# Kernel optimization log

Measured on AMD Instinct MI355X. Metric: run time of the kernel, lower is better.

## Reference

```python
import jax, jax.numpy as jnp
import numpy as np
import math

B, N, D, H, E, EDGE_DIM, GEO_DIM = 32, 256, 512, 8, 1024, 256, 64
HD = D // H

def _lin(x, W, b):
    return x @ W.T + b

def _ln(x, g, b):
    m = x.mean(-1, keepdims=True)
    v = ((x - m) ** 2).mean(-1, keepdims=True)
    return (x - m) * jax.lax.rsqrt(v + 1e-5) * g + b

def setup_inputs() -> dict:
    key = jax.random.key(0)
    ks = jax.random.split(key, 20)
    p = lambda k, s: jax.random.normal(k, s, jnp.float32) * 0.02
    inp = {
        'x': jax.random.normal(ks[0], (B, N, D), jnp.float32),
        'node_masks': jnp.ones((B, N), jnp.float32),
        'relation_edges': jax.random.randint(ks[1], (B, E, 2), 0, N),
        'relation_masks': (jax.random.uniform(ks[2], (B, E)) > 0.2).astype(jnp.float32),
        'relation_embeddings': jax.random.normal(ks[3], (B, E, EDGE_DIM), jnp.float32),
        'relation_geo_features': jax.random.normal(ks[4], (B, E, GEO_DIM), jnp.float32),
        'Wq': p(ks[5], (D, D)), 'bq': jnp.zeros((D,), jnp.float32),
        'Wk': p(ks[6], (D, D)), 'bk': jnp.zeros((D,), jnp.float32),
        'Wv': p(ks[7], (D, D)), 'bv': jnp.zeros((D,), jnp.float32),
        'W_eb': p(ks[8], (H, EDGE_DIM)), 'b_eb': jnp.zeros((H,), jnp.float32),
        'geo_ln_g': jnp.ones((GEO_DIM,), jnp.float32), 'geo_ln_b': jnp.zeros((GEO_DIM,), jnp.float32),
        'W_geo': p(ks[9], (H, GEO_DIM)), 'b_geo': jnp.zeros((H,), jnp.float32),
        'W_out': p(ks[10], (D, D)), 'b_out': jnp.zeros((D,), jnp.float32),
        'norm_g': jnp.ones((D,), jnp.float32), 'norm_b': jnp.zeros((D,), jnp.float32),
        'ff_ln_g': jnp.ones((D,), jnp.float32), 'ff_ln_b': jnp.zeros((D,), jnp.float32),
        'W_ff1': p(ks[11], (4 * D, D)), 'b_ff1': jnp.zeros((4 * D,), jnp.float32),
        'W_ff2': p(ks[12], (D, 4 * D)), 'b_ff2': jnp.zeros((D,), jnp.float32),
    }
    return inp

def reference(x, node_masks, relation_edges, relation_masks, relation_embeddings,
              relation_geo_features, Wq, bq, Wk, bk, Wv, bv, W_eb, b_eb,
              geo_ln_g, geo_ln_b, W_geo, b_geo, W_out, b_out, norm_g, norm_b,
              ff_ln_g, ff_ln_b, W_ff1, b_ff1, W_ff2, b_ff2):
    residual = x
    xn = _ln(x, norm_g, norm_b)
    q = _lin(xn, Wq, bq).reshape(B, N, H, HD)
    k = _lin(xn, Wk, bk).reshape(B, N, H, HD)
    v = _lin(xn, Wv, bv).reshape(B, N, H, HD)
    attn = jnp.einsum('bihd,bjhd->bhij', q, k) / math.sqrt(HD)

    nm = node_masks.astype(bool)
    pair_mask = nm[:, None, :, None] & nm[:, None, None, :]  # [B,1,N,N]

    valid = relation_masks.astype(bool)  # [B,E]
    idx = jnp.clip(relation_edges.astype(jnp.int32), 0, N - 1)
    src, dst = idx[..., 0], idx[..., 1]
    # route invalid edges to padding index N (sliced away after scatter)
    src_w = jnp.where(valid, src, N)
    dst_w = jnp.where(valid, dst, N)
    b_idx = jnp.broadcast_to(jnp.arange(B)[:, None], (B, E))

    adj = jnp.zeros((B, N + 1, N + 1), bool).at[:, :N, :N].set(jnp.eye(N, dtype=bool))
    adj = adj.at[b_idx, src_w, dst_w].set(True).at[b_idx, dst_w, src_w].set(True)
    rel_adj = adj[:, None, :N, :N]  # [B,1,N,N]

    eb = _lin(relation_embeddings, W_eb, b_eb)  # [B,E,H]
    gb = _lin(_ln(relation_geo_features, geo_ln_g, geo_ln_b), W_geo, b_geo)
    total_bias = (eb + gb).transpose(0, 2, 1)  # [B,H,E]
    bb = jnp.broadcast_to(b_idx[:, None, :], (B, H, E))
    hh = jnp.broadcast_to(jnp.arange(H)[None, :, None], (B, H, E))
    ss = jnp.broadcast_to(src_w[:, None, :], (B, H, E))
    dd = jnp.broadcast_to(dst_w[:, None, :], (B, H, E))
    rb = jnp.zeros((B, H, N + 1, N + 1), x.dtype)
    rb = rb.at[bb, hh, ss, dd].set(total_bias).at[bb, hh, dd, ss].set(total_bias)
    attn = attn + rb[:, :, :N, :N]

    mask = pair_mask & rel_adj
    attn = jnp.where(mask, attn, jnp.finfo(attn.dtype).min)
    attn = jnp.nan_to_num(jax.nn.softmax(attn, axis=-1))
    out = jnp.einsum('bhij,bjhd->bihd', attn, v).reshape(B, N, D)
    x2 = residual + _lin(out, W_out, b_out)
    h1 = jax.nn.silu(_lin(_ln(x2, ff_ln_g, ff_ln_b), W_ff1, b_ff1))
    x3 = x2 + _lin(h1, W_ff2, b_ff2)
    return x3 * node_masks[..., None]
```

## Files before the change

### kernel.cpp

```cpp
#include <hip/hip_runtime.h>

#define B_ 32
#define N_ 256
#define D_ 512
#define H_ 8
#define E_ 1024
#define HD_ 64

using u16 = unsigned short;
typedef short bf8_t __attribute__((ext_vector_type(8)));
typedef float f4_t __attribute__((ext_vector_type(4)));

__device__ __forceinline__ u16 f2bf(float f) {
  union { float f; unsigned u; } x; x.f = f;
  unsigned r = x.u + 0x7fffu + ((x.u >> 16) & 1u);
  return (u16)(r >> 16);
}
__device__ __forceinline__ f4_t mfma16(bf8_t a, bf8_t b, f4_t c) {
  return __builtin_amdgcn_mfma_f32_16x16x32_bf16(a, b, c, 0, 0, 0);
}
__device__ __forceinline__ void gload_lds16(const u16* g, u16* s) {
  __builtin_amdgcn_global_load_lds((const __attribute__((address_space(1))) void*)g,
                                   (__attribute__((address_space(3))) void*)s, 16, 0, 0);
}

__global__ __launch_bounds__(256) void cvt_all_kernel(
    const float* __restrict__ wq, const float* __restrict__ wk,
    const float* __restrict__ wv, const float* __restrict__ wo,
    const float* __restrict__ w1, const float* __restrict__ w2,
    u16* __restrict__ dq, u16* __restrict__ dk, u16* __restrict__ dv,
    u16* __restrict__ dox, u16* __restrict__ d1, u16* __restrict__ d2) {
  int blk = blockIdx.x;
  const float* src; u16* dst;
  if (blk < 256)        { src = wq; dst = dq; }
  else if (blk < 512)   { src = wk; dst = dk; blk -= 256; }
  else if (blk < 768)   { src = wv; dst = dv; blk -= 512; }
  else if (blk < 1024)  { src = wo; dst = dox; blk -= 768; }
  else if (blk < 2048)  { src = w1; dst = d1; blk -= 1024; }
  else                  { src = w2; dst = d2; blk -= 2048; }
  const int i = (blk * 256 + threadIdx.x) * 4;
  const float4 v = *(const float4*)(src + i);
  ushort4 o;
  o.x = f2bf(v.x); o.y = f2bf(v.y); o.z = f2bf(v.z); o.w = f2bf(v.w);
  *(ushort4*)(dst + i) = o;
}

__global__ __launch_bounds__(256) void ln_kernel(const float* __restrict__ x,
                                                 const float* __restrict__ g,
                                                 const float* __restrict__ bta,
                                                 u16* __restrict__ out) {
  const int row = blockIdx.x, t = threadIdx.x;
  const float* xr = x + (size_t)row * D_;
  float v0 = xr[t], v1 = xr[t + 256];
  float s = v0 + v1, ss = v0 * v0 + v1 * v1;
  #pragma unroll
  for (int m = 1; m < 64; m <<= 1) { s += __shfl_xor(s, m, 64); ss += __shfl_xor(ss, m, 64); }
  __shared__ float red[8];
  const int wave = t >> 6, lane = t & 63;
  if (!lane) { red[wave] = s; red[wave + 4] = ss; }
  __syncthreads();
  s = red[0] + red[1] + red[2] + red[3];
  ss = red[4] + red[5] + red[6] + red[7];
  const float mean = s * (1.f / D_);
  const float var = ss * (1.f / D_) - mean * mean;
  const float rs = rsqrtf(var + 1e-5f);
  out[(size_t)row * D_ + t] = f2bf((v0 - mean) * rs * g[t] + bta[t]);
  out[(size_t)row * D_ + t + 256] = f2bf((v1 - mean) * rs * g[t + 256] + bta[t + 256]);
}

__global__ __launch_bounds__(256) void geo_ln_kernel(const float* __restrict__ rgeo,
                                                     const float* __restrict__ g,
                                                     const float* __restrict__ b,
                                                     u16* __restrict__ gln) {
  const int wave = threadIdx.x >> 6, lane = threadIdx.x & 63;
  const int row = blockIdx.x * 4 + wave;
  const float gv = rgeo[(size_t)row * 64 + lane];
  float s = gv, ss = gv * gv;
  #pragma unroll
  for (int m = 1; m < 64; m <<= 1) { s += __shfl_xor(s, m, 64); ss += __shfl_xor(ss, m, 64); }
  const float mean = s * (1.f / 64.f);
  const float var = ss * (1.f / 64.f) - mean * mean;
  const float rs = rsqrtf(var + 1e-5f);
  gln[(size_t)row * 64 + lane] = f2bf((gv - mean) * rs * g[lane] + b[lane]);
}

__global__ __launch_bounds__(256) void edge_gemm_kernel(
    const float* __restrict__ remb, const u16* __restrict__ gln,
    const float* __restrict__ Web, const float* __restrict__ beb,
    const float* __restrict__ Wgeo, const float* __restrict__ bgeo,
    float* __restrict__ tb) {
  __shared__ u16 sWeb[16 * 256];
  __shared__ u16 sWgeo[16 * 64];
  const int t = threadIdx.x;
  for (int i = t; i < 2048; i += 256) { sWeb[i] = f2bf(Web[i]); sWeb[2048 + i] = 0; }
  for (int i = t; i < 512; i += 256)  { sWgeo[i] = f2bf(Wgeo[i]); sWgeo[512 + i] = 0; }
  __syncthreads();
  const int wave = t >> 6, lane = t & 63;
  const int am = lane & 15, quad = lane >> 4;
  const int e0 = blockIdx.x * 64 + wave * 16;

  f4_t acc = f4_t{0.f, 0.f, 0.f, 0.f};
  const float* ar = remb + (size_t)(e0 + am) * 256 + quad * 8;
  #pragma unroll
  for (int kt = 0; kt < 256; kt += 32) {
    const float4 p0 = *(const float4*)(ar + kt);
    const float4 p1 = *(const float4*)(ar + kt + 4);
    bf8_t a;
    a[0] = (short)f2bf(p0.x); a[1] = (short)f2bf(p0.y);
    a[2] = (short)f2bf(p0.z); a[3] = (short)f2bf(p0.w);
    a[4] = (short)f2bf(p1.x); a[5] = (short)f2bf(p1.y);
    a[6] = (short)f2bf(p1.z); a[7] = (short)f2bf(p1.w);
    const bf8_t bv = *(const bf8_t*)&sWeb[am * 256 + kt + quad * 8];
    acc = mfma16(a, bv, acc);
  }
  const u16* gr = gln + (size_t)(e0 + am) * 64 + quad * 8;
  #pragma unroll
  for (int kt = 0; kt < 64; kt += 32) {
    const bf8_t a2 = *(const bf8_t*)(gr + kt);
    const bf8_t bv2 = *(const bf8_t*)&sWgeo[am * 64 + kt + quad * 8];
    acc = mfma16(a2, bv2, acc);
  }
  if (am < 8) {
    const float bias_v = beb[am] + bgeo[am];
    #pragma unroll
    for (int r = 0; r < 4; ++r) {
      const int eg = e0 + quad * 4 + r;
      tb[(size_t)((eg >> 10) * H_ + am) * E_ + (eg & (E_ - 1))] = acc[r] + bias_v;
    }
  }
}

__global__ __launch_bounds__(256) void scatter_kernel(const int* __restrict__ edges,
                                                      const float* __restrict__ rmask,
                                                      int* __restrict__ win) {
  const int t = blockIdx.x * 256 + threadIdx.x;
  if (t >= B_ * E_) return;
  if (rmask[t] == 0.f) return;
  const int b = t >> 10, e = t & (E_ - 1);
  int s = edges[2 * t], d = edges[2 * t + 1];
  s = min(max(s, 0), N_ - 1);
  d = min(max(d, 0), N_ - 1);
  int* wb = win + (size_t)b * N_ * N_;
  atomicMax(&wb[s * N_ + d], e);
  atomicMax(&wb[d * N_ + s], E_ + e);
}

__global__ __launch_bounds__(256) void attn_kernel(
    const u16* __restrict__ q, const u16* __restrict__ k, const u16* __restrict__ vt,
    const float* __restrict__ tb, const int* __restrict__ win,
    const float* __restrict__ nm, u16* __restrict__ out) {
  __shared__ u16 swin[64 * 268];
  __shared__ float stb[E_];
  const int t = threadIdx.x;
  const int wave = t >> 6, lane = t & 63;
  const int am = lane & 15, quad = lane >> 4;
  const int qt = blockIdx.x, h = blockIdx.y, b = blockIdx.z;
  const int bh = b * H_ + h;
  const int q0 = qt * 64;

  ((float4*)stb)[t] = ((const float4*)(tb + (size_t)bh * E_))[t];
  {
    const int4* wsrc = (const int4*)(win + ((size_t)b * N_ + q0) * N_);
    #pragma unroll
    for (int kk = 0; kk < 16; ++kk) {
      const int g = kk * 256 + t;
      const int4 w4 = wsrc[g];
      ushort4 o;
      o.x = (u16)w4.x; o.y = (u16)w4.y; o.z = (u16)w4.z; o.w = (u16)w4.w;
      *(ushort4*)&swin[(g >> 6) * 268 + (g & 63) * 4] = o;
    }
  }

  f4_t sacc[16];
  #pragma unroll
  for (int j = 0; j < 16; ++j) sacc[j] = f4_t{0.f, 0.f, 0.f, 0.f};
  const u16* qbase = q + ((size_t)bh * N_ + q0 + wave * 16) * HD_;
  const bf8_t aq0 = *(const bf8_t*)&qbase[am * HD_ + quad * 8];
  const bf8_t aq1 = *(const bf8_t*)&qbase[am * HD_ + 32 + quad * 8];
  const u16* kbase = k + (size_t)bh * N_ * HD_;
  #pragma unroll
  for (int j = 0; j < 16; ++j) {
    const u16* kp = kbase + (size_t)(j * 16 + am) * HD_ + quad * 8;
    sacc[j] = mfma16(aq0, *(const bf8_t*)kp, sacc[j]);
    sacc[j] = mfma16(aq1, *(const bf8_t*)(kp + 32), sacc[j]);
  }
  __syncthreads();

  int lrow[4]; float nmr[4], rmax[4], rsum[4];
  #pragma unroll
  for (int r = 0; r < 4; ++r) {
    lrow[r] = wave * 16 + quad * 4 + r;
    nmr[r] = nm[b * N_ + q0 + lrow[r]];
    rmax[r] = -3.402823466e38f;
    rsum[r] = 0.f;
  }
  #pragma unroll
  for (int j = 0; j < 16; ++j) {
    const int cg = j * 16 + am;
    const float nmc = nm[b * N_ + cg];
    #pragma unroll
    for (int r = 0; r < 4; ++r) {
      const u16 w16 = swin[lrow[r] * 268 + cg];
      const bool has = (w16 != 0xFFFFu);
      const int idx = has ? ((w16 >= 1024) ? (w16 - 1024) : (int)w16) : 0;
      float s = sacc[j][r] * 0.125f;
      s += has ? stb[idx] : 0.f;
      const bool ok = (nmr[r] != 0.f) && (nmc != 0.f) && ((q0 + lrow[r]) == cg || has);
      s = ok ? s : -3.402823466e38f;
      sacc[j][r] = s;
      rmax[r] = fmaxf(rmax[r], s);
    }
  }
  #pragma unroll
  for (int m = 1; m < 16; m <<= 1)
    #pragma unroll
    for (int r = 0; r < 4; ++r) rmax[r] = fmaxf(rmax[r], __shfl_xor(rmax[r], m, 64));
  #pragma unroll
  for (int j = 0; j < 16; ++j)
    #pragma unroll
    for (int r = 0; r < 4; ++r) {
      const float e = __expf(sacc[j][r] - rmax[r]);
      sacc[j][r] = e;
      rsum[r] += e;
    }
  #pragma unroll
  for (int m = 1; m < 16; m <<= 1)
    #pragma unroll
    for (int r = 0; r < 4; ++r) rsum[r] += __shfl_xor(rsum[r], m, 64);
  float rinv[4];
  #pragma unroll
  for (int r = 0; r < 4; ++r) rinv[r] = 1.f / rsum[r];

  __syncthreads();
  u16* ps = swin + wave * 16 * 264;
  #pragma unroll
  for (int j = 0; j < 16; ++j)
    #pragma unroll
    for (int r = 0; r < 4; ++r)
      ps[(quad * 4 + r) * 264 + j * 16 + am] = f2bf(sacc[j][r] * rinv[r]);
  __syncthreads();

  f4_t oacc[4];
  #pragma unroll
  for (int t2 = 0; t2 < 4; ++t2) oacc[t2] = f4_t{0.f, 0.f, 0.f, 0.f};
  const u16* vb = vt + (size_t)bh * HD_ * N_;
  #pragma unroll
  for (int kc = 0; kc < 8; ++kc) {
    const bf8_t ap = *(const bf8_t*)&ps[am * 264 + kc * 32 + quad * 8];
    #pragma unroll
    for (int t2 = 0; t2 < 4; ++t2) {
      const u16* vp = vb + (size_t)(t2 * 16 + am) * N_ + kc * 32 + quad * 8;
      oacc[t2] = mfma16(ap, *(const bf8_t*)vp, oacc[t2]);
    }
  }
  #pragma unroll
  for (int t2 = 0; t2 < 4; ++t2)
    #pragma unroll
    for (int r = 0; r < 4; ++r) {
      const int n = q0 + wave * 16 + quad * 4 + r;
      const int d = t2 * 16 + am;
      out[((size_t)(b * N_ + n)) * D_ + h * HD_ + d] = f2bf(oacc[t2][r]);
    }
}

template <int MODE, int BN>
__global__ __launch_bounds__(256, 2) void gemm_k(
    const u16* __restrict__ A,
    const u16* __restrict__ W0, const u16* __restrict__ W1, const u16* __restrict__ W2,
    const float* __restrict__ b0, const float* __restrict__ b1, const float* __restrict__ b2,
    void* d0, void* d1, void* d2,
    const void* res, const float* __restrict__ nmask, int K) {
  constexpr int MJ = BN / 32;
  constexpr int CB = BN / 32;
  __shared__ u16 As[128 * 64];
  __shared__ u16 Bs[BN * 64];
  const int tid = threadIdx.x;
  const int wave = tid >> 6, lane = tid & 63;
  const int am = lane & 15, quad = lane >> 4;
  const int m0 = blockIdx.x * 128;
  int n0, proj = 0;
  const u16* W;
  const float* bias;
  if constexpr (MODE == 0) {
    proj = blockIdx.y >> 2;
    n0 = (blockIdx.y & 3) * BN;
    W = proj == 0 ? W0 : (proj == 1 ? W1 : W2);
    bias = proj == 0 ? b0 : (proj == 1 ? b1 : b2);
  } else {
    n0 = blockIdx.y * BN;
    W = W0;
    bias = b0;
  }
  const int wm = (wave >> 1) * 64;
  const int wn = (wave & 1) * (BN / 2);

  f4_t acc[4][MJ];
  #pragma unroll
  for (int i = 0; i < 4; ++i)
    #pragma unroll
    for (int j = 0; j < MJ; ++j) acc[i][j] = f4_t{0.f, 0.f, 0.f, 0.f};

  int arow[4], aq[4], brow[CB], bq[CB];
  #pragma unroll
  for (int c = 0; c < 4; ++c) {
    const int g = (wave * 4 + c) * 64 + lane;
    arow[c] = g >> 3;
    aq[c] = (g & 7) ^ (arow[c] & 7);
  }
  #pragma unroll
  for (int c = 0; c < CB; ++c) {
    const int g = (wave * CB + c) * 64 + lane;
    brow[c] = g >> 3;
    bq[c] = (g & 7) ^ (brow[c] & 7);
  }

  for (int kt = 0; kt < K; kt += 64) {
    #pragma unroll
    for (int c = 0; c < 4; ++c)
      gload_lds16(A + (size_t)(m0 + arow[c]) * K + kt + aq[c] * 8, &As[(wave * 4 + c) * 512]);
    #pragma unroll
    for (int c = 0; c < CB; ++c)
      gload_lds16(W + (size_t)(n0 + brow[c]) * K + kt + bq[c] * 8, &Bs[(wave * CB + c) * 512]);
    __syncthreads();
    #pragma unroll
    for (int kc = 0; kc < 2; ++kc) {
      bf8_t af[4], bfv[MJ];
      #pragma unroll
      for (int i = 0; i < 4; ++i) {
        const int r = wm + i * 16 + am;
        af[i] = *(const bf8_t*)&As[r * 64 + (((kc * 4 + quad) ^ (r & 7)) * 8)];
      }
      #pragma unroll
      for (int j = 0; j < MJ; ++j) {
        const int r = wn + j * 16 + am;
        bfv[j] = *(const bf8_t*)&Bs[r * 64 + (((kc * 4 + quad) ^ (r & 7)) * 8)];
      }
      #pragma unroll
      for (int i = 0; i < 4; ++i)
        #pragma unroll
        for (int j = 0; j < MJ; ++j) acc[i][j] = mfma16(af[i], bfv[j], acc[i][j]);
    }
    __syncthreads();
  }

  const int cb = n0 + wn + am;
  const int rb = m0 + wm + quad * 4;
  #pragma unroll
  for (int j = 0; j < MJ; ++j) {
    const int col = cb + j * 16;
    const float bv = bias[col];
    #pragma unroll
    for (int i = 0; i < 4; ++i) {
      #pragma unroll
      for (int r = 0; r < 4; ++r) {
        const int row = rb + i * 16 + r;
        float v = acc[i][j][r] + bv;
        if constexpr (MODE == 0) {
          const int b = row >> 8, n = row & (N_ - 1);
          const int h = col >> 6, hd = col & (HD_ - 1);
          u16* dst = (u16*)(proj == 0 ? d0 : (proj == 1 ? d1 : d2));
          const size_t idx = (proj < 2) ? (((size_t)(b * H_ + h) * N_ + n) * HD_ + hd)
                                        : (((size_t)(b * H_ + h) * HD_ + hd) * N_ + n);
          dst[idx] = f2bf(v);
        } else if constexpr (MODE == 2) {
          v += ((const float*)res)[(size_t)row * D_ + col];
          ((float*)d0)[(size_t)row * D_ + col] = v;
        } else if constexpr (MODE == 3) {
          v = v / (1.f + __expf(-v));
          ((u16*)d0)[(size_t)row * 2048 + col] = f2bf(v);
        } else {
          v += ((const float*)res)[(size_t)row * D_ + col];
          v *= nmask[row];
          ((float*)d0)[(size_t)row * D_ + col] = v;
        }
      }
    }
  }
}

extern "C" void kernel_launch(void* const* d_in, const int* in_sizes, int n_in,
                              void* d_out, int out_size, void* d_ws, size_t ws_size,
                              hipStream_t stream) {
  const float* x     = (const float*)d_in[0];
  const float* nm    = (const float*)d_in[1];
  const int*   edges = (const int*)d_in[2];
  const float* rmask = (const float*)d_in[3];
  const float* remb  = (const float*)d_in[4];
  const float* rgeo  = (const float*)d_in[5];
  const float* Wq = (const float*)d_in[6];  const float* bq = (const float*)d_in[7];
  const float* Wk = (const float*)d_in[8];  const float* bk = (const float*)d_in[9];
  const float* Wv = (const float*)d_in[10]; const float* bv = (const float*)d_in[11];
  const float* Web = (const float*)d_in[12]; const float* beb = (const float*)d_in[13];
  const float* glng = (const float*)d_in[14]; const float* glnb = (const float*)d_in[15];
  const float* Wgeo = (const float*)d_in[16]; const float* bgeo = (const float*)d_in[17];
  const float* Wout = (const float*)d_in[18]; const float* bout = (const float*)d_in[19];
  const float* ng = (const float*)d_in[20]; const float* nb = (const float*)d_in[21];
  const float* fg = (const float*)d_in[22]; const float* fb = (const float*)d_in[23];
  const float* Wff1 = (const float*)d_in[24]; const float* bff1 = (const float*)d_in[25];
  const float* Wff2 = (const float*)d_in[26]; const float* bff2 = (const float*)d_in[27];

  char* ws = (char*)d_ws;
  u16*   xn      = (u16*)(ws + 0);
  u16*   qb      = (u16*)(ws + 8388608);
  u16*   kb      = (u16*)(ws + 16777216);
  u16*   vtb     = (u16*)(ws + 25165824);
  u16*   h1      = (u16*)(ws + 0);
  u16*   gln     = (u16*)(ws + 0);
  int*   win     = (int*)(ws + 33554432);
  u16*   x2n     = (u16*)(ws + 33554432);
  float* tb      = (float*)(ws + 41943040);
  u16* Wq16   = (u16*)(ws + 42991616);
  u16* Wk16   = (u16*)(ws + 43515904);
  u16* Wv16   = (u16*)(ws + 44040192);
  u16* Wout16 = (u16*)(ws + 44564480);
  u16* Wff116 = (u16*)(ws + 45088768);
  u16* Wff216 = (u16*)(ws + 47185920);
  u16*   attnout = xn;
  float* out     = (float*)d_out;

  cvt_all_kernel<<<3072, 256, 0, stream>>>(Wq, Wk, Wv, Wout, Wff1, Wff2,
                                           Wq16, Wk16, Wv16, Wout16, Wff116, Wff216);
  hipMemsetAsync(win, 0xFF, (size_t)B_ * N_ * N_ * sizeof(int), stream);

  ln_kernel<<<B_ * N_, 256, 0, stream>>>(x, ng, nb, xn);
  gemm_k<0, 128><<<dim3(64, 12), 256, 0, stream>>>(xn, Wq16, Wk16, Wv16, bq, bk, bv,
                                                   (void*)qb, (void*)kb, (void*)vtb,
                                                   nullptr, nullptr, D_);
  scatter_kernel<<<(B_ * E_ + 255) / 256, 256, 0, stream>>>(edges, rmask, win);
  geo_ln_kernel<<<B_ * E_ / 4, 256, 0, stream>>>(rgeo, glng, glnb, gln);
  edge_gemm_kernel<<<B_ * E_ / 64, 256, 0, stream>>>(remb, gln, Web, beb, Wgeo, bgeo, tb);
  attn_kernel<<<dim3(N_ / 64, H_, B_), 256, 0, stream>>>(qb, kb, vtb, tb, win, nm, attnout);
  gemm_k<2, 64><<<dim3(64, 8), 256, 0, stream>>>(attnout, Wout16, nullptr, nullptr,
                                                 bout, nullptr, nullptr,
                                                 (void*)out, nullptr, nullptr,
                                                 (const void*)x, nullptr, D_);
  ln_kernel<<<B_ * N_, 256, 0, stream>>>(out, fg, fb, x2n);
  gemm_k<3, 128><<<dim3(64, 16), 256, 0, stream>>>(x2n, Wff116, nullptr, nullptr,
                                                   bff1, nullptr, nullptr,
                                                   (void*)h1, nullptr, nullptr, nullptr, nullptr, D_);
  gemm_k<4, 64><<<dim3(64, 8), 256, 0, stream>>>(h1, Wff216, nullptr, nullptr,
                                                 bff2, nullptr, nullptr,
                                                 (void*)out, nullptr, nullptr,
                                                 (const void*)out, nm, 2048);
}
```

Baseline: 326.3 us.

## Merge weight conversion, layernorm, scatter and edge-bias kernels into one prep launch

Combines the weight bf16 conversion, the input layernorm, the edge scatter and the edge-bias GEMM into a single kernel, dispatching on block index ranges. The geo layernorm is folded into the edge GEMM so each wave normalizes its rows in registers instead of writing and re-reading a bf16 intermediate. This removes four launches and one global round trip, at the cost of a heavier kernel whose shared-memory footprint applies to every block type.

```diff
diff --git a/kernel.cpp b/kernel.cpp
--- a/kernel.cpp
+++ b/kernel.cpp
@@ -24,25 +24,131 @@
                                    (__attribute__((address_space(3))) void*)s, 16, 0, 0);
 }
 
-__global__ __launch_bounds__(256) void cvt_all_kernel(
+__global__ __launch_bounds__(256) void prep_kernel(
     const float* __restrict__ wq, const float* __restrict__ wk,
     const float* __restrict__ wv, const float* __restrict__ wo,
     const float* __restrict__ w1, const float* __restrict__ w2,
     u16* __restrict__ dq, u16* __restrict__ dk, u16* __restrict__ dv,
-    u16* __restrict__ dox, u16* __restrict__ d1, u16* __restrict__ d2) {
-  int blk = blockIdx.x;
-  const float* src; u16* dst;
-  if (blk < 256)        { src = wq; dst = dq; }
-  else if (blk < 512)   { src = wk; dst = dk; blk -= 256; }
-  else if (blk < 768)   { src = wv; dst = dv; blk -= 512; }
-  else if (blk < 1024)  { src = wo; dst = dox; blk -= 768; }
-  else if (blk < 2048)  { src = w1; dst = d1; blk -= 1024; }
-  else                  { src = w2; dst = d2; blk -= 2048; }
-  const int i = (blk * 256 + threadIdx.x) * 4;
-  const float4 v = *(const float4*)(src + i);
-  ushort4 o;
-  o.x = f2bf(v.x); o.y = f2bf(v.y); o.z = f2bf(v.z); o.w = f2bf(v.w);
-  *(ushort4*)(dst + i) = o;
+    u16* __restrict__ dox, u16* __restrict__ d1, u16* __restrict__ d2,
+    const float* __restrict__ x, const float* __restrict__ ng,
+    const float* __restrict__ nb, u16* __restrict__ xn,
+    const int* __restrict__ edges, const float* __restrict__ rmask,
+    int* __restrict__ win,
+    const float* __restrict__ remb, const float* __restrict__ rgeo,
+    const float* __restrict__ Web, const float* __restrict__ beb,
+    const float* __restrict__ glng, const float* __restrict__ glnb,
+    const float* __restrict__ Wgeo, const float* __restrict__ bgeo,
+    float* __restrict__ tb) {
+  __shared__ float red[8];
+  __shared__ u16 sWeb[16 * 256];
+  __shared__ u16 sWgeo[16 * 64];
+  __shared__ float sLgb[128];
+  const int t = threadIdx.x;
+  const int blk0 = blockIdx.x;
+
+  if (blk0 < 3072) {
+    int blk = blk0;
+    const float* src; u16* dst;
+    if (blk < 256)        { src = wq; dst = dq; }
+    else if (blk < 512)   { src = wk; dst = dk; blk -= 256; }
+    else if (blk < 768)   { src = wv; dst = dv; blk -= 512; }
+    else if (blk < 1024)  { src = wo; dst = dox; blk -= 768; }
+    else if (blk < 2048)  { src = w1; dst = d1; blk -= 1024; }
+    else                  { src = w2; dst = d2; blk -= 2048; }
+    const int i = (blk * 256 + t) * 4;
+    const float4 v = *(const float4*)(src + i);
+    ushort4 o;
+    o.x = f2bf(v.x); o.y = f2bf(v.y); o.z = f2bf(v.z); o.w = f2bf(v.w);
+    *(ushort4*)(dst + i) = o;
+  } else if (blk0 < 11264) {
+    const int row = blk0 - 3072;
+    const float* xr = x + (size_t)row * D_;
+    float v0 = xr[t], v1 = xr[t + 256];
+    float s = v0 + v1, ss = v0 * v0 + v1 * v1;
+    #pragma unroll
+    for (int m = 1; m < 64; m <<= 1) { s += __shfl_xor(s, m, 64); ss += __shfl_xor(ss, m, 64); }
+    const int wave = t >> 6, lane = t & 63;
+    if (!lane) { red[wave] = s; red[wave + 4] = ss; }
+    __syncthreads();
+    s = red[0] + red[1] + red[2] + red[3];
+    ss = red[4] + red[5] + red[6] + red[7];
+    const float mean = s * (1.f / D_);
+    const float var = ss * (1.f / D_) - mean * mean;
+    const float rs = rsqrtf(var + 1e-5f);
+    xn[(size_t)row * D_ + t] = f2bf((v0 - mean) * rs * ng[t] + nb[t]);
+    xn[(size_t)row * D_ + t + 256] = f2bf((v1 - mean) * rs * ng[t + 256] + nb[t + 256]);
+  } else if (blk0 < 11392) {
+    const int idx = (blk0 - 11264) * 256 + t;
+    if (rmask[idx] != 0.f) {
+      const int b = idx >> 10, e = idx & (E_ - 1);
+      int s = edges[2 * idx], d = edges[2 * idx + 1];
+      s = min(max(s, 0), N_ - 1);
+      d = min(max(d, 0), N_ - 1);
+      int* wb = win + (size_t)b * N_ * N_;
+      atomicMax(&wb[s * N_ + d], e);
+      atomicMax(&wb[d * N_ + s], E_ + e);
+    }
+  } else {
+    const int eblk = blk0 - 11392;
+    for (int i = t; i < 2048; i += 256) { sWeb[i] = f2bf(Web[i]); sWeb[2048 + i] = 0; }
+    for (int i = t; i < 512; i += 256)  { sWgeo[i] = f2bf(Wgeo[i]); sWgeo[512 + i] = 0; }
+    if (t < 64) { sLgb[t] = glng[t]; sLgb[64 + t] = glnb[t]; }
+    __syncthreads();
+    const int wave = t >> 6, lane = t & 63;
+    const int am = lane & 15, quad = lane >> 4;
+    const int e0 = eblk * 64 + wave * 16;
+
+    f4_t acc = f4_t{0.f, 0.f, 0.f, 0.f};
+    const float* ar = remb + (size_t)(e0 + am) * 256 + quad * 8;
+    #pragma unroll
+    for (int kt = 0; kt < 256; kt += 32) {
+      const float4 p0 = *(const float4*)(ar + kt);
+      const float4 p1 = *(const float4*)(ar + kt + 4);
+      bf8_t a;
+      a[0] = (short)f2bf(p0.x); a[1] = (short)f2bf(p0.y);
+      a[2] = (short)f2bf(p0.z); a[3] = (short)f2bf(p0.w);
+      a[4] = (short)f2bf(p1.x); a[5] = (short)f2bf(p1.y);
+      a[6] = (short)f2bf(p1.z); a[7] = (short)f2bf(p1.w);
+      const bf8_t bv = *(const bf8_t*)&sWeb[am * 256 + kt + quad * 8];
+      acc = mfma16(a, bv, acc);
+    }
+    const float* gr = rgeo + (size_t)(e0 + am) * 64;
+    float v[16];
+    {
+      const float4 p0 = *(const float4*)(gr + quad * 8);
+      const float4 p1 = *(const float4*)(gr + quad * 8 + 4);
+      const float4 p2 = *(const float4*)(gr + 32 + quad * 8);
+      const float4 p3 = *(const float4*)(gr + 32 + quad * 8 + 4);
+      v[0] = p0.x; v[1] = p0.y; v[2] = p0.z; v[3] = p0.w;
+      v[4] = p1.x; v[5] = p1.y; v[6] = p1.z; v[7] = p1.w;
+      v[8] = p2.x; v[9] = p2.y; v[10] = p2.z; v[11] = p2.w;
+      v[12] = p3.x; v[13] = p3.y; v[14] = p3.z; v[15] = p3.w;
+    }
+    float s = 0.f, ss = 0.f;
+    #pragma unroll
+    for (int j = 0; j < 16; ++j) { s += v[j]; ss += v[j] * v[j]; }
+    s += __shfl_xor(s, 16, 64);  ss += __shfl_xor(ss, 16, 64);
+    s += __shfl_xor(s, 32, 64);  ss += __shfl_xor(ss, 32, 64);
+    const float mean = s * (1.f / 64.f);
+    const float rs = rsqrtf(ss * (1.f / 64.f) - mean * mean + 1e-5f);
+    bf8_t a2, a3;
+    #pragma unroll
+    for (int j = 0; j < 8; ++j) {
+      a2[j] = (short)f2bf((v[j] - mean) * rs * sLgb[quad * 8 + j] + sLgb[64 + quad * 8 + j]);
+      a3[j] = (short)f2bf((v[8 + j] - mean) * rs * sLgb[32 + quad * 8 + j] +
+                          sLgb[96 + quad * 8 + j]);
+    }
+    acc = mfma16(a2, *(const bf8_t*)&sWgeo[am * 64 + quad * 8], acc);
+    acc = mfma16(a3, *(const bf8_t*)&sWgeo[am * 64 + 32 + quad * 8], acc);
+    if (am < 8) {
+      const float bias_v = beb[am] + bgeo[am];
+      #pragma unroll
+      for (int r = 0; r < 4; ++r) {
+        const int eg = e0 + quad * 4 + r;
+        tb[(size_t)((eg >> 10) * H_ + am) * E_ + (eg & (E_ - 1))] = acc[r] + bias_v;
+      }
+    }
+  }
 }
 
 __global__ __launch_bounds__(256) void ln_kernel(const float* __restrict__ x,
@@ -66,83 +172,6 @@
   const float rs = rsqrtf(var + 1e-5f);
   out[(size_t)row * D_ + t] = f2bf((v0 - mean) * rs * g[t] + bta[t]);
   out[(size_t)row * D_ + t + 256] = f2bf((v1 - mean) * rs * g[t + 256] + bta[t + 256]);
-}
-
-__global__ __launch_bounds__(256) void geo_ln_kernel(const float* __restrict__ rgeo,
-                                                     const float* __restrict__ g,
-                                                     const float* __restrict__ b,
-                                                     u16* __restrict__ gln) {
-  const int wave = threadIdx.x >> 6, lane = threadIdx.x & 63;
-  const int row = blockIdx.x * 4 + wave;
-  const float gv = rgeo[(size_t)row * 64 + lane];
-  float s = gv, ss = gv * gv;
-  #pragma unroll
-  for (int m = 1; m < 64; m <<= 1) { s += __shfl_xor(s, m, 64); ss += __shfl_xor(ss, m, 64); }
-  const float mean = s * (1.f / 64.f);
-  const float var = ss * (1.f / 64.f) - mean * mean;
-  const float rs = rsqrtf(var + 1e-5f);
-  gln[(size_t)row * 64 + lane] = f2bf((gv - mean) * rs * g[lane] + b[lane]);
-}
-
-__global__ __launch_bounds__(256) void edge_gemm_kernel(
-    const float* __restrict__ remb, const u16* __restrict__ gln,
-    const float* __restrict__ Web, const float* __restrict__ beb,
-    const float* __restrict__ Wgeo, const float* __restrict__ bgeo,
-    float* __restrict__ tb) {
-  __shared__ u16 sWeb[16 * 256];
-  __shared__ u16 sWgeo[16 * 64];
-  const int t = threadIdx.x;
-  for (int i = t; i < 2048; i += 256) { sWeb[i] = f2bf(Web[i]); sWeb[2048 + i] = 0; }
-  for (int i = t; i < 512; i += 256)  { sWgeo[i] = f2bf(Wgeo[i]); sWgeo[512 + i] = 0; }
-  __syncthreads();
-  const int wave = t >> 6, lane = t & 63;
-  const int am = lane & 15, quad = lane >> 4;
-  const int e0 = blockIdx.x * 64 + wave * 16;
-
-  f4_t acc = f4_t{0.f, 0.f, 0.f, 0.f};
-  const float* ar = remb + (size_t)(e0 + am) * 256 + quad * 8;
-  #pragma unroll
-  for (int kt = 0; kt < 256; kt += 32) {
-    const float4 p0 = *(const float4*)(ar + kt);
-    const float4 p1 = *(const float4*)(ar + kt + 4);
-    bf8_t a;
-    a[0] = (short)f2bf(p0.x); a[1] = (short)f2bf(p0.y);
-    a[2] = (short)f2bf(p0.z); a[3] = (short)f2bf(p0.w);
-    a[4] = (short)f2bf(p1.x); a[5] = (short)f2bf(p1.y);
-    a[6] = (short)f2bf(p1.z); a[7] = (short)f2bf(p1.w);
-    const bf8_t bv = *(const bf8_t*)&sWeb[am * 256 + kt + quad * 8];
-    acc = mfma16(a, bv, acc);
-  }
-  const u16* gr = gln + (size_t)(e0 + am) * 64 + quad * 8;
-  #pragma unroll
-  for (int kt = 0; kt < 64; kt += 32) {
-    const bf8_t a2 = *(const bf8_t*)(gr + kt);
-    const bf8_t bv2 = *(const bf8_t*)&sWgeo[am * 64 + kt + quad * 8];
-    acc = mfma16(a2, bv2, acc);
-  }
-  if (am < 8) {
-    const float bias_v = beb[am] + bgeo[am];
-    #pragma unroll
-    for (int r = 0; r < 4; ++r) {
-      const int eg = e0 + quad * 4 + r;
-      tb[(size_t)((eg >> 10) * H_ + am) * E_ + (eg & (E_ - 1))] = acc[r] + bias_v;
-    }
-  }
-}
-
-__global__ __launch_bounds__(256) void scatter_kernel(const int* __restrict__ edges,
-                                                      const float* __restrict__ rmask,
-                                                      int* __restrict__ win) {
-  const int t = blockIdx.x * 256 + threadIdx.x;
-  if (t >= B_ * E_) return;
-  if (rmask[t] == 0.f) return;
-  const int b = t >> 10, e = t & (E_ - 1);
-  int s = edges[2 * t], d = edges[2 * t + 1];
-  s = min(max(s, 0), N_ - 1);
-  d = min(max(d, 0), N_ - 1);
-  int* wb = win + (size_t)b * N_ * N_;
-  atomicMax(&wb[s * N_ + d], e);
-  atomicMax(&wb[d * N_ + s], E_ + e);
 }
 
 __global__ __launch_bounds__(256) void attn_kernel(
@@ -405,7 +434,6 @@
   u16*   kb      = (u16*)(ws + 16777216);
   u16*   vtb     = (u16*)(ws + 25165824);
   u16*   h1      = (u16*)(ws + 0);
-  u16*   gln     = (u16*)(ws + 0);
   int*   win     = (int*)(ws + 33554432);
   u16*   x2n     = (u16*)(ws + 33554432);
   float* tb      = (float*)(ws + 41943040);
@@ -418,17 +446,15 @@
   u16*   attnout = xn;
   float* out     = (float*)d_out;
 
-  cvt_all_kernel<<<3072, 256, 0, stream>>>(Wq, Wk, Wv, Wout, Wff1, Wff2,
-                                           Wq16, Wk16, Wv16, Wout16, Wff116, Wff216);
   hipMemsetAsync(win, 0xFF, (size_t)B_ * N_ * N_ * sizeof(int), stream);
-
-  ln_kernel<<<B_ * N_, 256, 0, stream>>>(x, ng, nb, xn);
+  prep_kernel<<<11904, 256, 0, stream>>>(
+      Wq, Wk, Wv, Wout, Wff1, Wff2, Wq16, Wk16, Wv16, Wout16, Wff116, Wff216,
+      x, ng, nb, xn,
+      edges, rmask, win,
+      remb, rgeo, Web, beb, glng, glnb, Wgeo, bgeo, tb);
   gemm_k<0, 128><<<dim3(64, 12), 256, 0, stream>>>(xn, Wq16, Wk16, Wv16, bq, bk, bv,
                                                    (void*)qb, (void*)kb, (void*)vtb,
                                                    nullptr, nullptr, D_);
-  scatter_kernel<<<(B_ * E_ + 255) / 256, 256, 0, stream>>>(edges, rmask, win);
-  geo_ln_kernel<<<B_ * E_ / 4, 256, 0, stream>>>(rgeo, glng, glnb, gln);
-  edge_gemm_kernel<<<B_ * E_ / 64, 256, 0, stream>>>(remb, gln, Web, beb, Wgeo, bgeo, tb);
   attn_kernel<<<dim3(N_ / 64, H_, B_), 256, 0, stream>>>(qb, kb, vtb, tb, win, nm, attnout);
   gemm_k<2, 64><<<dim3(64, 8), 256, 0, stream>>>(attnout, Wout16, nullptr, nullptr,
                                                  bout, nullptr, nullptr,
```

Result: faster. 318.8 us (-2.3%).
